# Optimization experiments

Hardware: AMD Instinct MI355X
Metric: run time of the kernel (lower is better)

Reference implementation:

```python
import jax, jax.numpy as jnp
import numpy as np

N = 100000
E = 3200000
IN_C = 512
HID = 64
LOC = 64
GLOB = 64
OUT_C = 40
K = 10
ALPHA = 0.1


def setup_inputs() -> dict:
    key = jax.random.key(0)
    ks = jax.random.split(key, 10)
    batch_x = jax.random.normal(ks[0], (N, IN_C), dtype=jnp.float32)
    edge_index = jax.random.randint(ks[1], (2, E), 0, N, dtype=jnp.int32)
    glob_emb = jax.random.normal(ks[2], (N, GLOB), dtype=jnp.float32)
    # Linear params (Glorot-ish scale)
    W1 = jax.random.normal(ks[3], (IN_C, HID), dtype=jnp.float32) / np.sqrt(IN_C)
    b1 = jnp.zeros((HID,), dtype=jnp.float32)
    W2 = jax.random.normal(ks[4], (HID, LOC), dtype=jnp.float32) / np.sqrt(HID)
    b2 = jnp.zeros((LOC,), dtype=jnp.float32)
    # GPR-GNN PPR init coefficients: temp[k] = alpha*(1-alpha)^k, temp[K] = (1-alpha)^K
    temp_np = ALPHA * (1.0 - ALPHA) ** np.arange(K + 1)
    temp_np[-1] = (1.0 - ALPHA) ** K
    temp = jnp.asarray(temp_np, dtype=jnp.float32)
    Wl = jax.random.normal(ks[5], (LOC + GLOB, OUT_C), dtype=jnp.float32) / np.sqrt(LOC + GLOB)
    bl = jnp.zeros((OUT_C,), dtype=jnp.float32)
    return {"batch_x": batch_x, "edge_index": edge_index, "glob_emb": glob_emb,
            "W1": W1, "b1": b1, "W2": W2, "b2": b2, "temp": temp, "Wl": Wl, "bl": bl}


def _gcn_norm(edge_index, num_nodes):
    # add self loops (weight 1), symmetric normalization like PyG gcn_norm
    loops = jnp.arange(num_nodes, dtype=edge_index.dtype)
    row = jnp.concatenate([edge_index[0], loops])  # sources
    col = jnp.concatenate([edge_index[1], loops])  # targets
    w = jnp.ones(row.shape[0], dtype=jnp.float32)
    deg = jax.ops.segment_sum(w, col, num_segments=num_nodes)
    dinv = jnp.where(deg > 0, jax.lax.rsqrt(jnp.maximum(deg, 1.0)), 0.0)
    norm = dinv[row] * dinv[col]
    return row, col, norm


def reference(batch_x, edge_index, glob_emb, W1, b1, W2, b2, temp, Wl, bl):
    # eval mode: all dropouts are identity
    x = jax.nn.relu(batch_x @ W1 + b1)
    x = x @ W2 + b2  # [N, LOC]
    n = x.shape[0]
    row, col, norm = _gcn_norm(edge_index, n)
    hidden = x * temp[0]
    for k in range(K):
        # message: norm * x[src]; aggregate: scatter-add at target
        x = jax.ops.segment_sum(norm[:, None] * x[row], col, num_segments=n)
        hidden = hidden + temp[k + 1] * x
    emb = jnp.concatenate([hidden, glob_emb], axis=1)  # [N, LOC+GLOB]
    return emb @ Wl + bl
```

## Files before the change

kernel.cpp:

```cpp
#include <hip/hip_runtime.h>


typedef _Float16 half8 __attribute__((ext_vector_type(8)));


__global__ __launch_bounds__(256) void count_kernel(const int* __restrict__ edge,
                                                    int* __restrict__ counts, int E) {
  int e = blockIdx.x * 256 + threadIdx.x;
  if (e < E) atomicAdd(&counts[edge[E + e]], 1);
}

__global__ __launch_bounds__(256) void scanA_kernel(const int* __restrict__ counts,
                                                    int* __restrict__ incl,
                                                    int* __restrict__ partials, int Nn) {
  __shared__ int sbuf[256];
  int t = threadIdx.x;
  int base = blockIdx.x * 1024 + t * 4;
  int a0 = (base + 0 < Nn) ? counts[base + 0] : 0;
  int a1 = (base + 1 < Nn) ? counts[base + 1] : 0;
  int a2 = (base + 2 < Nn) ? counts[base + 2] : 0;
  int a3 = (base + 3 < Nn) ? counts[base + 3] : 0;
  int tot = a0 + a1 + a2 + a3;
  sbuf[t] = tot;
  __syncthreads();
  for (int off = 1; off < 256; off <<= 1) {
    int v = (t >= off) ? sbuf[t - off] : 0;
    __syncthreads();
    sbuf[t] += v;
    __syncthreads();
  }
  int excl = sbuf[t] - tot;
  if (base + 0 < Nn) incl[base + 0] = excl + a0;
  if (base + 1 < Nn) incl[base + 1] = excl + a0 + a1;
  if (base + 2 < Nn) incl[base + 2] = excl + a0 + a1 + a2;
  if (base + 3 < Nn) incl[base + 3] = excl + tot;
  if (t == 255) partials[blockIdx.x] = sbuf[255];
}

__global__ void scanB_kernel(const int* __restrict__ partials,
                             int* __restrict__ chunkoff, int B) {
  __shared__ int sbuf[256];
  int t = threadIdx.x;
  int v = (t < B) ? partials[t] : 0;
  sbuf[t] = v;
  __syncthreads();
  for (int off = 1; off < 256; off <<= 1) {
    int u = (t >= off) ? sbuf[t - off] : 0;
    __syncthreads();
    sbuf[t] += u;
    __syncthreads();
  }
  chunkoff[t] = sbuf[t] - v;
}

__global__ __launch_bounds__(256) void finalize_scan_kernel(const int* __restrict__ incl,
                                                            const int* __restrict__ chunkoff,
                                                            int* __restrict__ rowptr, int Nn) {
  int i = blockIdx.x * 256 + threadIdx.x;
  if (i < Nn) rowptr[i + 1] = incl[i] + chunkoff[i >> 10];
  if (i == 0) rowptr[0] = 0;
}

__global__ __launch_bounds__(256) void dinv_kernel(const int* __restrict__ counts,
                                                   float* __restrict__ dinv, int Nn) {
  int i = blockIdx.x * 256 + threadIdx.x;
  if (i < Nn) dinv[i] = rsqrtf((float)(counts[i] + 1));
}

__global__ __launch_bounds__(256) void fill_kernel(const int* __restrict__ edge,
                                                   const int* __restrict__ rowptr,
                                                   int* __restrict__ cursor,
                                                   int* __restrict__ srcoff, int E) {
  int e = blockIdx.x * 256 + threadIdx.x;
  if (e < E) {
    int r = edge[e];
    int c = edge[E + e];
    int p = rowptr[c] + atomicAdd(&cursor[c], 1);
    srcoff[p] = r * 128;
  }
}


__global__ __launch_bounds__(256) void mlp1_kernel(const float* __restrict__ X,
                                                   const float* __restrict__ W1,
                                                   const float* __restrict__ b1,
                                                   float* __restrict__ H, int Nn) {
  __shared__ float sXT[64][68];
  __shared__ float sW[64][68];
  int t = threadIdx.x;
  int m0 = blockIdx.x * 64;
  int tx = t & 15, ty = t >> 4;
  float acc[4][4];
#pragma unroll
  for (int i = 0; i < 4; ++i)
#pragma unroll
    for (int j = 0; j < 4; ++j) acc[i][j] = 0.f;

  for (int k0 = 0; k0 < 512; k0 += 64) {
#pragma unroll
    for (int i = 0; i < 4; ++i) {
      int lin = t + i * 256;
      int m = lin >> 4;
      int kq = lin & 15;
      int gr = m0 + m;
      float4 v = make_float4(0.f, 0.f, 0.f, 0.f);
      if (gr < Nn) v = *(const float4*)&X[(size_t)gr * 512 + k0 + kq * 4];
      sXT[kq * 4 + 0][m] = v.x;
      sXT[kq * 4 + 1][m] = v.y;
      sXT[kq * 4 + 2][m] = v.z;
      sXT[kq * 4 + 3][m] = v.w;
    }
#pragma unroll
    for (int i = 0; i < 4; ++i) {
      int lin = t + i * 256;
      int k = lin >> 4;
      int nq = lin & 15;
      float4 v = *(const float4*)&W1[(size_t)(k0 + k) * 64 + nq * 4];
      *(float4*)&sW[k][nq * 4] = v;
    }
    __syncthreads();
#pragma unroll 8
    for (int kk = 0; kk < 64; ++kk) {
      float4 a = *(const float4*)&sXT[kk][ty * 4];
      float4 b = *(const float4*)&sW[kk][tx * 4];
      float av[4] = {a.x, a.y, a.z, a.w};
      float bv[4] = {b.x, b.y, b.z, b.w};
#pragma unroll
      for (int i = 0; i < 4; ++i)
#pragma unroll
        for (int j = 0; j < 4; ++j) acc[i][j] += av[i] * bv[j];
    }
    __syncthreads();
  }
  float4 bb = *(const float4*)&b1[tx * 4];
  float bvv[4] = {bb.x, bb.y, bb.z, bb.w};
#pragma unroll
  for (int i = 0; i < 4; ++i) {
    int r = m0 + ty * 4 + i;
    if (r < Nn) {
      float4 o;
      o.x = fmaxf(acc[i][0] + bvv[0], 0.f);
      o.y = fmaxf(acc[i][1] + bvv[1], 0.f);
      o.z = fmaxf(acc[i][2] + bvv[2], 0.f);
      o.w = fmaxf(acc[i][3] + bvv[3], 0.f);
      *(float4*)&H[(size_t)r * 64 + tx * 4] = o;
    }
  }
}


__global__ void computeM_kernel(const float* __restrict__ W2, const float* __restrict__ Wl,
                                const float* __restrict__ b2, float* __restrict__ Mm,
                                float* __restrict__ cv) {
  int t = threadIdx.x;
  for (int idx = t; idx < 2560; idx += 256) {
    int k = idx / 40, o = idx - k * 40;
    float s = 0.f;
    for (int j = 0; j < 64; ++j) s += W2[k * 64 + j] * Wl[j * 40 + o];
    Mm[idx] = s;
  }
  if (t < 40) {
    float s = 0.f;
    for (int j = 0; j < 64; ++j) s += b2[j] * Wl[j * 40 + t];
    cv[t] = s;
  }
}

__global__ void zeropad_kernel(char* __restrict__ yA, char* __restrict__ yB, int Nn) {
  int t = threadIdx.x;
  ((_Float16*)(yA + (size_t)Nn * 128))[t] = (_Float16)0.f;
  ((_Float16*)(yB + (size_t)Nn * 128))[t] = (_Float16)0.f;
}


__global__ __launch_bounds__(256) void z0_kernel(const float* __restrict__ H,
                                                 const float* __restrict__ Mm,
                                                 const float* __restrict__ cv,
                                                 const float* __restrict__ dinv,
                                                 const float* __restrict__ temp,
                                                 char* __restrict__ y0,
                                                 float* __restrict__ hid, int Nn) {
  __shared__ float sM[2624];
  __shared__ float sc[40];
  int t = threadIdx.x;
  for (int i = t; i < 2560; i += 256) sM[i] = Mm[i];
  for (int i = 2560 + t; i < 2624; i += 256) sM[i] = 0.f;
  if (t < 40) sc[t] = cv[t];
  __syncthreads();
  int wid = t >> 6, lane = t & 63;
  int node = blockIdx.x * 4 + wid;
  if (node < Nn) {
    float h = H[(size_t)node * 64 + lane];
    float acc = (lane < 40) ? sc[lane] : 0.f;
#pragma unroll 8
    for (int k = 0; k < 64; ++k) acc += __shfl(h, k) * sM[k * 40 + lane];
    if (lane < 40) {
      float di = dinv[node];
      float y = di * acc;
      ((_Float16*)(y0 + (size_t)node * 128))[lane] = (_Float16)y;
      hid[(size_t)node * 40 + lane] = temp[0] * y;
    }
  }
}


__global__ __launch_bounds__(256) void prop_kernel(const char* __restrict__ yin,
                                                   char* __restrict__ yout,
                                                   float* __restrict__ hid,
                                                   const int* __restrict__ srcoff,
                                                   const int* __restrict__ rowptr,
                                                   const float* __restrict__ dinv,
                                                   const float* __restrict__ temp,
                                                   int kidx, int Nn) {
  __shared__ float red[4][60][8];
  int t = threadIdx.x, wid = t >> 6, lane = t & 63;
  int node = blockIdx.x * 4 + wid;
  int sub = lane / 5;
  int cl = lane - sub * 5;
  const int zoff = Nn * 128;
  float a0 = 0.f, a1 = 0.f, a2 = 0.f, a3 = 0.f, a4 = 0.f, a5 = 0.f, a6 = 0.f, a7 = 0.f;
  if (node < Nn) {
    int start = rowptr[node], end = rowptr[node + 1];
    int claneoff = cl << 4;
    for (int b0 = start; b0 < end; b0 += 60) {
      int j = b0 + lane;
      int moff = (lane < 60 && j < end) ? srcoff[j] : zoff;
      int rem = end - b0;
      int cnt = rem < 60 ? rem : 60;
      int tmax = (cnt + 11) / 12;
      for (int tt = 0; tt < tmax; ++tt) {
        int off = __shfl(moff, tt * 12 + sub);
        half8 v = *(const half8*)(yin + off + claneoff);
        a0 += (float)v[0]; a1 += (float)v[1]; a2 += (float)v[2]; a3 += (float)v[3];
        a4 += (float)v[4]; a5 += (float)v[5]; a6 += (float)v[6]; a7 += (float)v[7];
      }
    }
  }
  if (lane < 60) {
    red[wid][lane][0] = a0; red[wid][lane][1] = a1;
    red[wid][lane][2] = a2; red[wid][lane][3] = a3;
    red[wid][lane][4] = a4; red[wid][lane][5] = a5;
    red[wid][lane][6] = a6; red[wid][lane][7] = a7;
  }
  __syncthreads();
  if (node < Nn && lane < 5) {
    float s[8];
#pragma unroll
    for (int i = 0; i < 8; ++i) s[i] = 0.f;
#pragma unroll
    for (int g = 0; g < 12; ++g)
#pragma unroll
      for (int i = 0; i < 8; ++i) s[i] += red[wid][g * 5 + lane][i];
    float di = dinv[node];
    float m = di * di;
    half8 self = *(const half8*)(yin + (size_t)node * 128 + (lane << 4));
    float yn[8];
    half8 outv;
#pragma unroll
    for (int i = 0; i < 8; ++i) {
      yn[i] = m * (s[i] + (float)self[i]);
      outv[i] = (_Float16)yn[i];
    }
    *(half8*)(yout + (size_t)node * 128 + (lane << 4)) = outv;
    float tk = temp[kidx];
    float* hp = &hid[(size_t)node * 40 + lane * 8];
    float4 h0 = *(float4*)hp;
    float4 h1 = *(float4*)(hp + 4);
    h0.x += tk * yn[0]; h0.y += tk * yn[1]; h0.z += tk * yn[2]; h0.w += tk * yn[3];
    h1.x += tk * yn[4]; h1.y += tk * yn[5]; h1.z += tk * yn[6]; h1.w += tk * yn[7];
    *(float4*)hp = h0;
    *(float4*)(hp + 4) = h1;
  }
}


__global__ __launch_bounds__(256) void final_kernel(const float* __restrict__ glob,
                                                    const float* __restrict__ Wl,
                                                    const float* __restrict__ bl,
                                                    const float* __restrict__ hid,
                                                    const int* __restrict__ counts,
                                                    const float* __restrict__ dinv,
                                                    float* __restrict__ out, int Nn) {
  __shared__ float sW[2624];
  __shared__ float sb[40];
  int t = threadIdx.x;
  for (int i = t; i < 2560; i += 256) sW[i] = Wl[2560 + i];
  for (int i = 2560 + t; i < 2624; i += 256) sW[i] = 0.f;
  if (t < 40) sb[t] = bl[t];
  __syncthreads();
  int wid = t >> 6, lane = t & 63;
  int node = blockIdx.x * 4 + wid;
  if (node < Nn) {
    float g = glob[(size_t)node * 64 + lane];
    float acc = (lane < 40) ? sb[lane] : 0.f;
#pragma unroll 8
    for (int k = 0; k < 64; ++k) acc += __shfl(g, k) * sW[k * 40 + lane];
    if (lane < 40) {
      float sc = (float)(counts[node] + 1) * dinv[node];
      out[(size_t)node * 40 + lane] = sc * hid[(size_t)node * 40 + lane] + acc;
    }
  }
}


extern "C" void kernel_launch(void* const* d_in, const int* in_sizes, int n_in,
                              void* d_out, int out_size, void* d_ws, size_t ws_size,
                              hipStream_t stream) {
  const float* X    = (const float*)d_in[0];
  const int*   edge = (const int*)d_in[1];
  const float* glob = (const float*)d_in[2];
  const float* W1   = (const float*)d_in[3];
  const float* b1   = (const float*)d_in[4];
  const float* W2   = (const float*)d_in[5];
  const float* b2   = (const float*)d_in[6];
  const float* temp = (const float*)d_in[7];
  const float* Wl   = (const float*)d_in[8];
  const float* bl   = (const float*)d_in[9];
  float* out = (float*)d_out;

  int Nn = in_sizes[0] / 512;
  int E  = in_sizes[1] / 2;
  int Kk = in_sizes[7] - 1;

  char* p = (char*)d_ws;
  auto alloc = [&](size_t bytes) {
    char* r = p;
    p += (bytes + 255) & ~(size_t)255;
    return r;
  };
  int*   counts   = (int*)alloc((size_t)Nn * 4);
  int*   rowptr   = (int*)alloc((size_t)(Nn + 1) * 4);
  int*   incl     = (int*)alloc((size_t)Nn * 4);
  int*   partials = (int*)alloc(256 * 4);
  int*   chunkoff = (int*)alloc(256 * 4);
  int*   cursor   = (int*)alloc((size_t)Nn * 4);
  float* dinv     = (float*)alloc((size_t)Nn * 4);
  int*   srcoff   = (int*)alloc((size_t)E * 4);
  float* Hbuf     = (float*)alloc((size_t)Nn * 64 * 4);
  float* Mm       = (float*)alloc(2560 * 4);
  float* cv       = (float*)alloc(64 * 4);
  char*  yA       = (char*)alloc((size_t)(Nn + 1) * 128);
  char*  yB       = (char*)alloc((size_t)(Nn + 1) * 128);
  float* hid      = (float*)alloc((size_t)Nn * 40 * 4);

  hipMemsetAsync(counts, 0, (size_t)Nn * 4, stream);
  hipMemsetAsync(cursor, 0, (size_t)Nn * 4, stream);

  count_kernel<<<(E + 255) / 256, 256, 0, stream>>>(edge, counts, E);
  int B = (Nn + 1023) / 1024;
  scanA_kernel<<<B, 256, 0, stream>>>(counts, incl, partials, Nn);
  scanB_kernel<<<1, 256, 0, stream>>>(partials, chunkoff, B);
  finalize_scan_kernel<<<(Nn + 255) / 256, 256, 0, stream>>>(incl, chunkoff, rowptr, Nn);
  dinv_kernel<<<(Nn + 255) / 256, 256, 0, stream>>>(counts, dinv, Nn);
  fill_kernel<<<(E + 255) / 256, 256, 0, stream>>>(edge, rowptr, cursor, srcoff, E);

  mlp1_kernel<<<(Nn + 63) / 64, 256, 0, stream>>>(X, W1, b1, Hbuf, Nn);
  computeM_kernel<<<1, 256, 0, stream>>>(W2, Wl, b2, Mm, cv);
  zeropad_kernel<<<1, 64, 0, stream>>>(yA, yB, Nn);

  int nodeBlocks = (Nn + 3) / 4;
  z0_kernel<<<nodeBlocks, 256, 0, stream>>>(Hbuf, Mm, cv, dinv, temp, yA, hid, Nn);

  char* yin = yA;
  char* yout = yB;
  for (int k = 1; k <= Kk; ++k) {
    prop_kernel<<<nodeBlocks, 256, 0, stream>>>(yin, yout, hid, srcoff, rowptr, dinv,
                                                temp, k, Nn);
    char* tmpp = yin; yin = yout; yout = tmpp;
  }

  final_kernel<<<nodeBlocks, 256, 0, stream>>>(glob, Wl, bl, hid, counts, dinv, out, Nn);
}
```

Baseline: 1.444 ms.

## Split propagated features into 64B and 16B planes, propagate each in separate blocks

The 40-channel fp16 propagation state moves from one 128-byte-padded row per node to two tightly packed planes: 32 channels in 64-byte rows and 8 channels in 16-byte rows. The propagation kernel launches twice as many blocks. The first half gathers the 64-byte plane with 4 lanes per neighbor, and the second half gathers the 16-byte plane with one lane per neighbor and a shuffle reduction. This is meant to cut padded gather traffic and cache footprint and to use all 64 lanes. The cost is reading the neighbor list twice and running extra blocks.

```diff
diff --git a/kernel.cpp b/kernel.cpp
--- a/kernel.cpp
+++ b/kernel.cpp
@@ -70,13 +70,13 @@
 __global__ __launch_bounds__(256) void fill_kernel(const int* __restrict__ edge,
                                                    const int* __restrict__ rowptr,
                                                    int* __restrict__ cursor,
-                                                   int* __restrict__ srcoff, int E) {
+                                                   int* __restrict__ srcidx, int E) {
   int e = blockIdx.x * 256 + threadIdx.x;
   if (e < E) {
     int r = edge[e];
     int c = edge[E + e];
     int p = rowptr[c] + atomicAdd(&cursor[c], 1);
-    srcoff[p] = r * 128;
+    srcidx[p] = r;
   }
 }
 
@@ -166,10 +166,17 @@
   }
 }
 
-__global__ void zeropad_kernel(char* __restrict__ yA, char* __restrict__ yB, int Nn) {
-  int t = threadIdx.x;
-  ((_Float16*)(yA + (size_t)Nn * 128))[t] = (_Float16)0.f;
-  ((_Float16*)(yB + (size_t)Nn * 128))[t] = (_Float16)0.f;
+__global__ void zeropad_kernel(char* __restrict__ yAa, char* __restrict__ yAb,
+                               char* __restrict__ yBa, char* __restrict__ yBb, int Nn) {
+  int t = threadIdx.x;
+  if (t < 32) {
+    ((_Float16*)(yAa + (size_t)Nn * 64))[t] = (_Float16)0.f;
+    ((_Float16*)(yBa + (size_t)Nn * 64))[t] = (_Float16)0.f;
+  }
+  if (t < 8) {
+    ((_Float16*)(yAb + (size_t)Nn * 16))[t] = (_Float16)0.f;
+    ((_Float16*)(yBb + (size_t)Nn * 16))[t] = (_Float16)0.f;
+  }
 }
 
 
@@ -178,7 +185,8 @@
                                                  const float* __restrict__ cv,
                                                  const float* __restrict__ dinv,
                                                  const float* __restrict__ temp,
-                                                 char* __restrict__ y0,
+                                                 char* __restrict__ y0a,
+                                                 char* __restrict__ y0b,
                                                  float* __restrict__ hid, int Nn) {
   __shared__ float sM[2624];
   __shared__ float sc[40];
@@ -197,79 +205,122 @@
     if (lane < 40) {
       float di = dinv[node];
       float y = di * acc;
-      ((_Float16*)(y0 + (size_t)node * 128))[lane] = (_Float16)y;
+      if (lane < 32)
+        ((_Float16*)(y0a + (size_t)node * 64))[lane] = (_Float16)y;
+      else
+        ((_Float16*)(y0b + (size_t)node * 16))[lane - 32] = (_Float16)y;
       hid[(size_t)node * 40 + lane] = temp[0] * y;
     }
   }
 }
 
 
-__global__ __launch_bounds__(256) void prop_kernel(const char* __restrict__ yin,
-                                                   char* __restrict__ yout,
+__global__ __launch_bounds__(256) void prop_kernel(const char* __restrict__ yin_a,
+                                                   const char* __restrict__ yin_b,
+                                                   char* __restrict__ yout_a,
+                                                   char* __restrict__ yout_b,
                                                    float* __restrict__ hid,
-                                                   const int* __restrict__ srcoff,
+                                                   const int* __restrict__ srcidx,
                                                    const int* __restrict__ rowptr,
                                                    const float* __restrict__ dinv,
                                                    const float* __restrict__ temp,
-                                                   int kidx, int Nn) {
-  __shared__ float red[4][60][8];
+                                                   int kidx, int Nn, int nodeBlocks) {
+  __shared__ float red[4][64][8];
   int t = threadIdx.x, wid = t >> 6, lane = t & 63;
-  int node = blockIdx.x * 4 + wid;
-  int sub = lane / 5;
-  int cl = lane - sub * 5;
-  const int zoff = Nn * 128;
-  float a0 = 0.f, a1 = 0.f, a2 = 0.f, a3 = 0.f, a4 = 0.f, a5 = 0.f, a6 = 0.f, a7 = 0.f;
-  if (node < Nn) {
-    int start = rowptr[node], end = rowptr[node + 1];
+  if ((int)blockIdx.x < nodeBlocks) {
+    int node = blockIdx.x * 4 + wid;
+    int sub = lane >> 2, cl = lane & 3;
     int claneoff = cl << 4;
-    for (int b0 = start; b0 < end; b0 += 60) {
-      int j = b0 + lane;
-      int moff = (lane < 60 && j < end) ? srcoff[j] : zoff;
-      int rem = end - b0;
-      int cnt = rem < 60 ? rem : 60;
-      int tmax = (cnt + 11) / 12;
-      for (int tt = 0; tt < tmax; ++tt) {
-        int off = __shfl(moff, tt * 12 + sub);
-        half8 v = *(const half8*)(yin + off + claneoff);
-        a0 += (float)v[0]; a1 += (float)v[1]; a2 += (float)v[2]; a3 += (float)v[3];
-        a4 += (float)v[4]; a5 += (float)v[5]; a6 += (float)v[6]; a7 += (float)v[7];
+    float a[8];
+#pragma unroll
+    for (int i = 0; i < 8; ++i) a[i] = 0.f;
+    if (node < Nn) {
+      int start = rowptr[node], end = rowptr[node + 1];
+      for (int b0 = start; b0 < end; b0 += 64) {
+        int j = b0 + lane;
+        int idx = (j < end) ? srcidx[j] : Nn;
+        int rem = end - b0;
+        int cnt = rem < 64 ? rem : 64;
+        int tmax = (cnt + 15) >> 4;
+        for (int tt = 0; tt < tmax; ++tt) {
+          int s = __shfl(idx, tt * 16 + sub);
+          half8 v = *(const half8*)(yin_a + (size_t)s * 64 + claneoff);
+#pragma unroll
+          for (int i = 0; i < 8; ++i) a[i] += (float)v[i];
+        }
       }
     }
-  }
-  if (lane < 60) {
-    red[wid][lane][0] = a0; red[wid][lane][1] = a1;
-    red[wid][lane][2] = a2; red[wid][lane][3] = a3;
-    red[wid][lane][4] = a4; red[wid][lane][5] = a5;
-    red[wid][lane][6] = a6; red[wid][lane][7] = a7;
-  }
-  __syncthreads();
-  if (node < Nn && lane < 5) {
-    float s[8];
-#pragma unroll
-    for (int i = 0; i < 8; ++i) s[i] = 0.f;
-#pragma unroll
-    for (int g = 0; g < 12; ++g)
-#pragma unroll
-      for (int i = 0; i < 8; ++i) s[i] += red[wid][g * 5 + lane][i];
-    float di = dinv[node];
-    float m = di * di;
-    half8 self = *(const half8*)(yin + (size_t)node * 128 + (lane << 4));
-    float yn[8];
-    half8 outv;
-#pragma unroll
-    for (int i = 0; i < 8; ++i) {
-      yn[i] = m * (s[i] + (float)self[i]);
-      outv[i] = (_Float16)yn[i];
-    }
-    *(half8*)(yout + (size_t)node * 128 + (lane << 4)) = outv;
-    float tk = temp[kidx];
-    float* hp = &hid[(size_t)node * 40 + lane * 8];
-    float4 h0 = *(float4*)hp;
-    float4 h1 = *(float4*)(hp + 4);
-    h0.x += tk * yn[0]; h0.y += tk * yn[1]; h0.z += tk * yn[2]; h0.w += tk * yn[3];
-    h1.x += tk * yn[4]; h1.y += tk * yn[5]; h1.z += tk * yn[6]; h1.w += tk * yn[7];
-    *(float4*)hp = h0;
-    *(float4*)(hp + 4) = h1;
+#pragma unroll
+    for (int i = 0; i < 8; ++i) red[wid][lane][i] = a[i];
+    __syncthreads();
+    if (node < Nn && lane < 4) {
+      float s[8];
+#pragma unroll
+      for (int i = 0; i < 8; ++i) s[i] = 0.f;
+#pragma unroll
+      for (int g = 0; g < 16; ++g)
+#pragma unroll
+        for (int i = 0; i < 8; ++i) s[i] += red[wid][g * 4 + lane][i];
+      float di = dinv[node];
+      float m = di * di;
+      half8 self = *(const half8*)(yin_a + (size_t)node * 64 + (lane << 4));
+      float yn[8];
+      half8 outv;
+#pragma unroll
+      for (int i = 0; i < 8; ++i) {
+        yn[i] = m * (s[i] + (float)self[i]);
+        outv[i] = (_Float16)yn[i];
+      }
+      *(half8*)(yout_a + (size_t)node * 64 + (lane << 4)) = outv;
+      float tk = temp[kidx];
+      float* hp = &hid[(size_t)node * 40 + lane * 8];
+      float4 h0 = *(float4*)hp;
+      float4 h1 = *(float4*)(hp + 4);
+      h0.x += tk * yn[0]; h0.y += tk * yn[1]; h0.z += tk * yn[2]; h0.w += tk * yn[3];
+      h1.x += tk * yn[4]; h1.y += tk * yn[5]; h1.z += tk * yn[6]; h1.w += tk * yn[7];
+      *(float4*)hp = h0;
+      *(float4*)(hp + 4) = h1;
+    }
+  } else {
+    int node = (blockIdx.x - nodeBlocks) * 4 + wid;
+    if (node < Nn) {
+      float a[8];
+#pragma unroll
+      for (int i = 0; i < 8; ++i) a[i] = 0.f;
+      int start = rowptr[node], end = rowptr[node + 1];
+      for (int b0 = start; b0 < end; b0 += 64) {
+        int j = b0 + lane;
+        int idx = (j < end) ? srcidx[j] : Nn;
+        half8 v = *(const half8*)(yin_b + (size_t)idx * 16);
+#pragma unroll
+        for (int i = 0; i < 8; ++i) a[i] += (float)v[i];
+      }
+#pragma unroll
+      for (int d = 32; d >= 1; d >>= 1)
+#pragma unroll
+        for (int i = 0; i < 8; ++i) a[i] += __shfl_xor(a[i], d);
+      if (lane == 0) {
+        float di = dinv[node];
+        float m = di * di;
+        half8 self = *(const half8*)(yin_b + (size_t)node * 16);
+        float yn[8];
+        half8 outv;
+#pragma unroll
+        for (int i = 0; i < 8; ++i) {
+          yn[i] = m * (a[i] + (float)self[i]);
+          outv[i] = (_Float16)yn[i];
+        }
+        *(half8*)(yout_b + (size_t)node * 16) = outv;
+        float tk = temp[kidx];
+        float* hp = &hid[(size_t)node * 40 + 32];
+        float4 h0 = *(float4*)hp;
+        float4 h1 = *(float4*)(hp + 4);
+        h0.x += tk * yn[0]; h0.y += tk * yn[1]; h0.z += tk * yn[2]; h0.w += tk * yn[3];
+        h1.x += tk * yn[4]; h1.y += tk * yn[5]; h1.z += tk * yn[6]; h1.w += tk * yn[7];
+        *(float4*)hp = h0;
+        *(float4*)(hp + 4) = h1;
+      }
+    }
   }
 }
 
@@ -335,12 +386,14 @@
   int*   chunkoff = (int*)alloc(256 * 4);
   int*   cursor   = (int*)alloc((size_t)Nn * 4);
   float* dinv     = (float*)alloc((size_t)Nn * 4);
-  int*   srcoff   = (int*)alloc((size_t)E * 4);
+  int*   srcidx   = (int*)alloc((size_t)E * 4);
   float* Hbuf     = (float*)alloc((size_t)Nn * 64 * 4);
   float* Mm       = (float*)alloc(2560 * 4);
   float* cv       = (float*)alloc(64 * 4);
-  char*  yA       = (char*)alloc((size_t)(Nn + 1) * 128);
-  char*  yB       = (char*)alloc((size_t)(Nn + 1) * 128);
+  char*  yAa      = (char*)alloc((size_t)(Nn + 1) * 64);
+  char*  yBa      = (char*)alloc((size_t)(Nn + 1) * 64);
+  char*  yAb      = (char*)alloc((size_t)(Nn + 1) * 16);
+  char*  yBb      = (char*)alloc((size_t)(Nn + 1) * 16);
   float* hid      = (float*)alloc((size_t)Nn * 40 * 4);
 
   hipMemsetAsync(counts, 0, (size_t)Nn * 4, stream);
@@ -352,21 +405,23 @@
   scanB_kernel<<<1, 256, 0, stream>>>(partials, chunkoff, B);
   finalize_scan_kernel<<<(Nn + 255) / 256, 256, 0, stream>>>(incl, chunkoff, rowptr, Nn);
   dinv_kernel<<<(Nn + 255) / 256, 256, 0, stream>>>(counts, dinv, Nn);
-  fill_kernel<<<(E + 255) / 256, 256, 0, stream>>>(edge, rowptr, cursor, srcoff, E);
+  fill_kernel<<<(E + 255) / 256, 256, 0, stream>>>(edge, rowptr, cursor, srcidx, E);
 
   mlp1_kernel<<<(Nn + 63) / 64, 256, 0, stream>>>(X, W1, b1, Hbuf, Nn);
   computeM_kernel<<<1, 256, 0, stream>>>(W2, Wl, b2, Mm, cv);
-  zeropad_kernel<<<1, 64, 0, stream>>>(yA, yB, Nn);
+  zeropad_kernel<<<1, 64, 0, stream>>>(yAa, yAb, yBa, yBb, Nn);
 
   int nodeBlocks = (Nn + 3) / 4;
-  z0_kernel<<<nodeBlocks, 256, 0, stream>>>(Hbuf, Mm, cv, dinv, temp, yA, hid, Nn);
-
-  char* yin = yA;
-  char* yout = yB;
+  z0_kernel<<<nodeBlocks, 256, 0, stream>>>(Hbuf, Mm, cv, dinv, temp, yAa, yAb, hid, Nn);
+
+  char* yina = yAa; char* yinb = yAb;
+  char* youta = yBa; char* youtb = yBb;
   for (int k = 1; k <= Kk; ++k) {
-    prop_kernel<<<nodeBlocks, 256, 0, stream>>>(yin, yout, hid, srcoff, rowptr, dinv,
-                                                temp, k, Nn);
-    char* tmpp = yin; yin = yout; yout = tmpp;
+    prop_kernel<<<2 * nodeBlocks, 256, 0, stream>>>(yina, yinb, youta, youtb, hid,
+                                                    srcidx, rowptr, dinv, temp, k, Nn,
+                                                    nodeBlocks);
+    char* ta = yina; yina = youta; youta = ta;
+    char* tb = yinb; yinb = youtb; youtb = tb;
   }
 
   final_kernel<<<nodeBlocks, 256, 0, stream>>>(glob, Wl, bl, hid, counts, dinv, out, Nn);
```

Measured after the change: 1.827 ms. 26.5% more time.
